# Performance work log

Measured on AMD Instinct MI355X. Metric: run time of the kernel, lower is better.

Reference implementation:

```python
import jax, jax.numpy as jnp
import numpy as np

BS, GRID, LSTM_H, CNN_C, PROJ = 256, 49, 512, 2048, 512


def setup_inputs() -> dict:
    key = jax.random.key(0)
    ks = jax.random.split(key, 7)
    s = lambda fan_in: 1.0 / np.sqrt(fan_in)
    return {
        "lstm_hidden": jax.random.normal(ks[0], (BS, LSTM_H), jnp.float32),
        "cnn_feat": jax.random.normal(ks[1], (BS, GRID, CNN_C), jnp.float32),
        "W_lstm": jax.random.normal(ks[2], (PROJ, LSTM_H), jnp.float32) * s(LSTM_H),
        "b_lstm": jax.random.normal(ks[3], (PROJ,), jnp.float32) * s(LSTM_H),
        "W_cnn": jax.random.normal(ks[4], (PROJ, CNN_C), jnp.float32) * s(CNN_C),
        "b_cnn": jax.random.normal(ks[5], (PROJ,), jnp.float32) * s(CNN_C),
        "w_attn": jax.random.normal(ks[6], (1, PROJ), jnp.float32) * s(PROJ),
    }


def reference(lstm_hidden, cnn_feat, W_lstm, b_lstm, W_cnn, b_cnn, w_attn):
    # H computed once (original loop recomputes it per grid, identically)
    H = lstm_hidden @ W_lstm.T + b_lstm                       # (bs, P)
    V = jnp.einsum("bgc,pc->bgp", cnn_feat, W_cnn) + b_cnn    # (bs, G, P)
    z = jnp.tanh(H[:, None, :] + V) @ w_attn[0]               # (bs, G)
    bs, G = z.shape
    # Faithful to torch: cat over grids along dim 0 -> (G*bs,), then view(bs, G)
    z_scrambled = jnp.swapaxes(z, 0, 1).reshape(bs, G)
    return jax.nn.softmax(z_scrambled, axis=1)
```

## Files before the change

### kernel.cpp

```cpp
#include <hip/hip_runtime.h>
#include <math.h>

#define BSZ    256
#define GRID_N 49
#define LSTMH  512
#define CNN_C  2048
#define PROJ   512
#define KAUG   2560
#define M_TOT  12544
#define MT     64
#define NT     256
#define BK     64
#define KTILES (KAUG / BK)
#define NBLK   ((M_TOT / MT) * (PROJ / NT))

typedef short bf16x8 __attribute__((ext_vector_type(8)));
typedef float f32x4  __attribute__((ext_vector_type(4)));

static __device__ __forceinline__ unsigned short bf16_rne(float f) {
    unsigned int u = __float_as_uint(f);
    u = u + 0x7FFFu + ((u >> 16) & 1u);
    return (unsigned short)(u >> 16);
}
static __device__ __forceinline__ uint4 pack8f(const float* f) {
    uint4 o;
    o.x = (unsigned int)bf16_rne(f[0]) | ((unsigned int)bf16_rne(f[1]) << 16);
    o.y = (unsigned int)bf16_rne(f[2]) | ((unsigned int)bf16_rne(f[3]) << 16);
    o.z = (unsigned int)bf16_rne(f[4]) | ((unsigned int)bf16_rne(f[5]) << 16);
    o.w = (unsigned int)bf16_rne(f[6]) | ((unsigned int)bf16_rne(f[7]) << 16);
    return o;
}
static __device__ __forceinline__ float tanh_fast(float x) {
    float e = __expf(2.f * x);
    return 1.f - 2.f / (e + 1.f);
}
static __device__ __forceinline__ void glds16(const void* g, void* l) {
    __builtin_amdgcn_global_load_lds(
        (const __attribute__((address_space(1))) unsigned int*)g,
        (__attribute__((address_space(3))) unsigned int*)l, 16, 0, 0);
}

__global__ __launch_bounds__(256) void prep_w(const float* __restrict__ Wc,
                                              const float* __restrict__ Wl,
                                              unsigned short* __restrict__ wsW) {
    int c  = blockIdx.x * 256 + threadIdx.x;
    int p  = c / 320;
    int kc = (c % 320) * 8;
    const float* src = (kc < CNN_C) ? (Wc + (size_t)p * CNN_C + kc)
                                    : (Wl + (size_t)p * LSTMH + (kc - CNN_C));
    float f[8];
    *(float4*)&f[0] = ((const float4*)src)[0];
    *(float4*)&f[4] = ((const float4*)src)[1];
    *(uint4*)(wsW + (size_t)p * KAUG + kc) = pack8f(f);
}

template <bool WS>
__global__ __launch_bounds__(256, 2) void gemm_k(
    const float* __restrict__ lstm, const float* __restrict__ cnn,
    const float* __restrict__ Wc,   const float* __restrict__ Wl,
    const float* __restrict__ bl,   const float* __restrict__ bc,
    const float* __restrict__ wat,  const unsigned short* __restrict__ wsW,
    float* __restrict__ out)
{
    __shared__ unsigned short Ash[MT][BK];
    __shared__ unsigned short Bsh[NT][BK];
    __shared__ float zp[4][MT];

    const int t   = threadIdx.x;
    const int w   = t >> 6;
    const int l   = t & 63;
    const int q   = l >> 4;
    const int r16 = l & 15;

    const int m0 = (int)(blockIdx.x >> 1) * MT;
    const int n0 = (int)(blockIdx.x & 1) * NT;

    const int ra  = t >> 2;
    const int ca0 = t & 3;
    const int sa  = ra & 7;
    const int grow = m0 + ra;
    const int ab   = grow / 49;
    const int ag   = grow - ab * 49;
    const float* cnnb  = cnn + ((size_t)ab * GRID_N + ag) * CNN_C;
    const float* lstmb = lstm + (size_t)ab * LSTMH;

    f32x4 acc[4][4];
    #pragma unroll
    for (int mt = 0; mt < 4; ++mt)
        #pragma unroll
        for (int nt = 0; nt < 4; ++nt)
            acc[mt][nt] = (f32x4){0.f, 0.f, 0.f, 0.f};

    float4 fa0, fa1, fa2, fa3;

    auto a_load = [&](int k0) {
        const float* s = (k0 < CNN_C) ? (cnnb + k0) : (lstmb + (k0 - CNN_C));
        const float4* p0 = (const float4*)(s + ca0 * 8);
        const float4* p1 = (const float4*)(s + (ca0 + 4) * 8);
        fa0 = p0[0]; fa1 = p0[1];
        fa2 = p1[0]; fa3 = p1[1];
    };
    auto a_write = [&]() {
        float f[8];
        *(float4*)&f[0] = fa0; *(float4*)&f[4] = fa1;
        *(uint4*)&Ash[ra][(ca0 ^ sa) * 8] = pack8f(f);
        *(float4*)&f[0] = fa2; *(float4*)&f[4] = fa3;
        *(uint4*)&Ash[ra][((ca0 + 4) ^ sa) * 8] = pack8f(f);
    };
    auto b_stage = [&](int k0) {
        if constexpr (WS) {
            const int rsub = l >> 3;
            const int cg   = (l & 7) ^ rsub;
            #pragma unroll
            for (int j = 0; j < 8; ++j) {
                const int rowb = w * 64 + j * 8;
                const unsigned short* g =
                    wsW + (size_t)(n0 + rowb + rsub) * KAUG + k0 + cg * 8;
                glds16(g, &Bsh[rowb][0]);
            }
        } else {
            const float* s = (k0 < CNN_C) ? (Wc + (size_t)(n0 + t) * CNN_C + k0)
                                          : (Wl + (size_t)(n0 + t) * LSTMH + (k0 - CNN_C));
            const int sw = t & 7;
            #pragma unroll
            for (int c = 0; c < 8; ++c) {
                float f[8];
                *(float4*)&f[0] = ((const float4*)(s + c * 8))[0];
                *(float4*)&f[4] = ((const float4*)(s + c * 8))[1];
                *(uint4*)&Bsh[t][(c ^ sw) * 8] = pack8f(f);
            }
        }
    };

    a_load(0);
    a_write();
    b_stage(0);

    for (int kt = 0; kt < KTILES; ++kt) {
        __syncthreads();
        const bool more = (kt + 1 < KTILES);
        if (more) a_load((kt + 1) * BK);
        #pragma unroll
        for (int ks = 0; ks < 2; ++ks) {
            const int cp = ((ks * 4 + q) ^ (r16 & 7)) * 8;
            bf16x8 af[4], bfr[4];
            #pragma unroll
            for (int mt = 0; mt < 4; ++mt)
                af[mt] = *(const bf16x8*)&Ash[mt * 16 + r16][cp];
            #pragma unroll
            for (int nt = 0; nt < 4; ++nt)
                bfr[nt] = *(const bf16x8*)&Bsh[w * 64 + nt * 16 + r16][cp];
            #pragma unroll
            for (int mt = 0; mt < 4; ++mt)
                #pragma unroll
                for (int nt = 0; nt < 4; ++nt)
                    acc[mt][nt] = __builtin_amdgcn_mfma_f32_16x16x32_bf16(
                        af[mt], bfr[nt], acc[mt][nt], 0, 0, 0);
        }
        __syncthreads();
        if (more) { a_write(); b_stage((kt + 1) * BK); }
    }

    float part[4][4];
    #pragma unroll
    for (int mt = 0; mt < 4; ++mt)
        #pragma unroll
        for (int rr = 0; rr < 4; ++rr) part[mt][rr] = 0.f;
    #pragma unroll
    for (int nt = 0; nt < 4; ++nt) {
        const int p = n0 + w * 64 + nt * 16 + r16;
        const float bb = bl[p] + bc[p];
        const float wa = wat[p];
        #pragma unroll
        for (int mt = 0; mt < 4; ++mt)
            #pragma unroll
            for (int rr = 0; rr < 4; ++rr)
                part[mt][rr] += tanh_fast(acc[mt][nt][rr] + bb) * wa;
    }
    #pragma unroll
    for (int mt = 0; mt < 4; ++mt)
        #pragma unroll
        for (int rr = 0; rr < 4; ++rr) {
            float v = part[mt][rr];
            v += __shfl_xor(v, 1);
            v += __shfl_xor(v, 2);
            v += __shfl_xor(v, 4);
            v += __shfl_xor(v, 8);
            if (r16 == 0) zp[w][mt * 16 + q * 4 + rr] = v;
        }
    __syncthreads();
    if (t < MT) {
        const float v = zp[0][t] + zp[1][t] + zp[2][t] + zp[3][t];
        const int row = m0 + t;
        const int b2  = row / 49;
        const int g2  = row - b2 * 49;
        atomicAdd(&out[g2 * BSZ + b2], v);
    }
}

__global__ __launch_bounds__(64) void softmax_rows(float* __restrict__ out)
{
    const int i = blockIdx.x;
    const int j = threadIdx.x;
    float x = (j < GRID_N) ? out[i * GRID_N + j] : -1e30f;
    float m = x;
    #pragma unroll
    for (int off = 32; off > 0; off >>= 1) m = fmaxf(m, __shfl_xor(m, off));
    float e = (j < GRID_N) ? __expf(x - m) : 0.f;
    float s = e;
    #pragma unroll
    for (int off = 32; off > 0; off >>= 1) s += __shfl_xor(s, off);
    if (j < GRID_N) out[i * GRID_N + j] = e / s;
}

extern "C" void kernel_launch(void* const* d_in, const int* in_sizes, int n_in,
                              void* d_out, int out_size, void* d_ws, size_t ws_size,
                              hipStream_t stream)
{
    const float* lstm = (const float*)d_in[0];
    const float* cnn  = (const float*)d_in[1];
    const float* Wl   = (const float*)d_in[2];
    const float* bl   = (const float*)d_in[3];
    const float* Wc   = (const float*)d_in[4];
    const float* bc   = (const float*)d_in[5];
    const float* wat  = (const float*)d_in[6];
    float* out = (float*)d_out;

    hipMemsetAsync(out, 0, (size_t)out_size * sizeof(float), stream);

    const size_t wneed = (size_t)PROJ * KAUG * sizeof(unsigned short);
    if (ws_size >= wneed) {
        unsigned short* wsW = (unsigned short*)d_ws;
        prep_w<<<dim3(640), dim3(256), 0, stream>>>(Wc, Wl, wsW);
        gemm_k<true><<<dim3(NBLK), dim3(256), 0, stream>>>(lstm, cnn, Wc, Wl, bl, bc, wat, wsW, out);
    } else {
        gemm_k<false><<<dim3(NBLK), dim3(256), 0, stream>>>(lstm, cnn, Wc, Wl, bl, bc, wat, nullptr, out);
    }
    softmax_rows<<<dim3(BSZ), dim3(64), 0, stream>>>(out);
}
```

Before: 231.7 us.

## Halve N tile, load B fragments directly to registers, double-buffer A in LDS

The N tile drops from 256 to 128, so four blocks share each M tile and each wave owns 32 columns. B is no longer staged through LDS via global_load_lds. Each lane loads its bf16 weight fragments straight from global memory into a two-stage register buffer. A is double-buffered in LDS with a ping-pong loop unrolled by two, which drops one barrier per k-tile. Occupancy is raised to 3 blocks per SM, at the cost of reading the converted activations (A) twice as often and doing uncoalesced per-lane B loads.

```diff
diff --git a/kernel.cpp b/kernel.cpp
--- a/kernel.cpp
+++ b/kernel.cpp
@@ -9,7 +9,7 @@
 #define KAUG   2560
 #define M_TOT  12544
 #define MT     64
-#define NT     256
+#define NT     128
 #define BK     64
 #define KTILES (KAUG / BK)
 #define NBLK   ((M_TOT / MT) * (PROJ / NT))
@@ -33,11 +33,6 @@
 static __device__ __forceinline__ float tanh_fast(float x) {
     float e = __expf(2.f * x);
     return 1.f - 2.f / (e + 1.f);
-}
-static __device__ __forceinline__ void glds16(const void* g, void* l) {
-    __builtin_amdgcn_global_load_lds(
-        (const __attribute__((address_space(1))) unsigned int*)g,
-        (__attribute__((address_space(3))) unsigned int*)l, 16, 0, 0);
 }
 
 __global__ __launch_bounds__(256) void prep_w(const float* __restrict__ Wc,
@@ -55,15 +50,14 @@
 }
 
 template <bool WS>
-__global__ __launch_bounds__(256, 2) void gemm_k(
+__global__ __launch_bounds__(256, 3) void gemm_k(
     const float* __restrict__ lstm, const float* __restrict__ cnn,
     const float* __restrict__ Wc,   const float* __restrict__ Wl,
     const float* __restrict__ bl,   const float* __restrict__ bc,
     const float* __restrict__ wat,  const unsigned short* __restrict__ wsW,
     float* __restrict__ out)
 {
-    __shared__ unsigned short Ash[MT][BK];
-    __shared__ unsigned short Bsh[NT][BK];
+    __shared__ unsigned short Ash[2][MT][BK];
     __shared__ float zp[4][MT];
 
     const int t   = threadIdx.x;
@@ -72,93 +66,100 @@
     const int q   = l >> 4;
     const int r16 = l & 15;
 
-    const int m0 = (int)(blockIdx.x >> 1) * MT;
-    const int n0 = (int)(blockIdx.x & 1) * NT;
-
-    const int ra  = t >> 2;
-    const int ca0 = t & 3;
-    const int sa  = ra & 7;
+    const int m0 = (int)(blockIdx.x >> 2) * MT;
+    const int n0 = (int)(blockIdx.x & 3) * NT;
+
+    const int ra = t >> 2;
+    const int ca = t & 3;
+    const int sw = ra & 7;
     const int grow = m0 + ra;
     const int ab   = grow / 49;
     const int ag   = grow - ab * 49;
     const float* cnnb  = cnn + ((size_t)ab * GRID_N + ag) * CNN_C;
     const float* lstmb = lstm + (size_t)ab * LSTMH;
 
-    f32x4 acc[4][4];
+    const int bn = n0 + w * 32 + r16;
+    const int bk = q * 8;
+
+    f32x4 acc[4][2];
     #pragma unroll
     for (int mt = 0; mt < 4; ++mt)
         #pragma unroll
-        for (int nt = 0; nt < 4; ++nt)
+        for (int nt = 0; nt < 2; ++nt)
             acc[mt][nt] = (f32x4){0.f, 0.f, 0.f, 0.f};
 
-    float4 fa0, fa1, fa2, fa3;
+    float4 fa[4];
+    bf16x8 Breg[2][2][2];
 
     auto a_load = [&](int k0) {
         const float* s = (k0 < CNN_C) ? (cnnb + k0) : (lstmb + (k0 - CNN_C));
-        const float4* p0 = (const float4*)(s + ca0 * 8);
-        const float4* p1 = (const float4*)(s + (ca0 + 4) * 8);
-        fa0 = p0[0]; fa1 = p0[1];
-        fa2 = p1[0]; fa3 = p1[1];
-    };
-    auto a_write = [&]() {
-        float f[8];
-        *(float4*)&f[0] = fa0; *(float4*)&f[4] = fa1;
-        *(uint4*)&Ash[ra][(ca0 ^ sa) * 8] = pack8f(f);
-        *(float4*)&f[0] = fa2; *(float4*)&f[4] = fa3;
-        *(uint4*)&Ash[ra][((ca0 + 4) ^ sa) * 8] = pack8f(f);
-    };
-    auto b_stage = [&](int k0) {
-        if constexpr (WS) {
-            const int rsub = l >> 3;
-            const int cg   = (l & 7) ^ rsub;
-            #pragma unroll
-            for (int j = 0; j < 8; ++j) {
-                const int rowb = w * 64 + j * 8;
-                const unsigned short* g =
-                    wsW + (size_t)(n0 + rowb + rsub) * KAUG + k0 + cg * 8;
-                glds16(g, &Bsh[rowb][0]);
+        const float4* p = (const float4*)(s + ca * 16);
+        fa[0] = p[0]; fa[1] = p[1]; fa[2] = p[2]; fa[3] = p[3];
+    };
+    auto a_write = [&](int buf) {
+        float f[16];
+        *(float4*)&f[0]  = fa[0]; *(float4*)&f[4]  = fa[1];
+        *(float4*)&f[8]  = fa[2]; *(float4*)&f[12] = fa[3];
+        *(uint4*)&Ash[buf][ra][((2 * ca) ^ sw) * 8]     = pack8f(&f[0]);
+        *(uint4*)&Ash[buf][ra][((2 * ca + 1) ^ sw) * 8] = pack8f(&f[8]);
+    };
+    auto b_load = [&](int k0, int pp) {
+        #pragma unroll
+        for (int nt = 0; nt < 2; ++nt)
+            #pragma unroll
+            for (int ks = 0; ks < 2; ++ks) {
+                if constexpr (WS) {
+                    Breg[pp][nt][ks] = *(const bf16x8*)(
+                        wsW + (size_t)(bn + nt * 16) * KAUG + k0 + ks * 32 + bk);
+                } else {
+                    const int kk = k0 + ks * 32 + bk;
+                    const int n  = bn + nt * 16;
+                    const float* s = (kk < CNN_C) ? (Wc + (size_t)n * CNN_C + kk)
+                                                  : (Wl + (size_t)n * LSTMH + (kk - CNN_C));
+                    float f[8];
+                    *(float4*)&f[0] = ((const float4*)s)[0];
+                    *(float4*)&f[4] = ((const float4*)s)[1];
+                    uint4 u = pack8f(f);
+                    Breg[pp][nt][ks] = *(bf16x8*)&u;
+                }
             }
-        } else {
-            const float* s = (k0 < CNN_C) ? (Wc + (size_t)(n0 + t) * CNN_C + k0)
-                                          : (Wl + (size_t)(n0 + t) * LSTMH + (k0 - CNN_C));
-            const int sw = t & 7;
-            #pragma unroll
-            for (int c = 0; c < 8; ++c) {
-                float f[8];
-                *(float4*)&f[0] = ((const float4*)(s + c * 8))[0];
-                *(float4*)&f[4] = ((const float4*)(s + c * 8))[1];
-                *(uint4*)&Bsh[t][(c ^ sw) * 8] = pack8f(f);
-            }
-        }
-    };
-
-    a_load(0);
-    a_write();
-    b_stage(0);
-
-    for (int kt = 0; kt < KTILES; ++kt) {
-        __syncthreads();
-        const bool more = (kt + 1 < KTILES);
-        if (more) a_load((kt + 1) * BK);
+    };
+    auto compute = [&](int buf, int pp) {
         #pragma unroll
         for (int ks = 0; ks < 2; ++ks) {
             const int cp = ((ks * 4 + q) ^ (r16 & 7)) * 8;
-            bf16x8 af[4], bfr[4];
+            bf16x8 af[4];
             #pragma unroll
             for (int mt = 0; mt < 4; ++mt)
-                af[mt] = *(const bf16x8*)&Ash[mt * 16 + r16][cp];
-            #pragma unroll
-            for (int nt = 0; nt < 4; ++nt)
-                bfr[nt] = *(const bf16x8*)&Bsh[w * 64 + nt * 16 + r16][cp];
+                af[mt] = *(const bf16x8*)&Ash[buf][mt * 16 + r16][cp];
             #pragma unroll
             for (int mt = 0; mt < 4; ++mt)
                 #pragma unroll
-                for (int nt = 0; nt < 4; ++nt)
+                for (int nt = 0; nt < 2; ++nt)
                     acc[mt][nt] = __builtin_amdgcn_mfma_f32_16x16x32_bf16(
-                        af[mt], bfr[nt], acc[mt][nt], 0, 0, 0);
+                        af[mt], Breg[pp][nt][ks], acc[mt][nt], 0, 0, 0);
         }
+    };
+
+    a_load(0);
+    b_load(0, 0);
+    a_write(0);
+    __syncthreads();
+
+    for (int kt = 0; kt < KTILES; kt += 2) {
+        a_load((kt + 1) * BK);
+        b_load((kt + 1) * BK, 1);
+        compute(0, 0);
+        a_write(1);
         __syncthreads();
-        if (more) { a_write(); b_stage((kt + 1) * BK); }
+        const bool more = (kt + 2 < KTILES);
+        if (more) {
+            a_load((kt + 2) * BK);
+            b_load((kt + 2) * BK, 0);
+        }
+        compute(1, 1);
+        if (more) a_write(0);
+        __syncthreads();
     }
 
     float part[4][4];
@@ -167,8 +168,8 @@
         #pragma unroll
         for (int rr = 0; rr < 4; ++rr) part[mt][rr] = 0.f;
     #pragma unroll
-    for (int nt = 0; nt < 4; ++nt) {
-        const int p = n0 + w * 64 + nt * 16 + r16;
+    for (int nt = 0; nt < 2; ++nt) {
+        const int p = n0 + w * 32 + nt * 16 + r16;
         const float bb = bl[p] + bc[p];
         const float wa = wat[p];
         #pragma unroll
```

Result: slower. 283.2 us (+22.3%).

## Double the K tile and register-prefetch B instead of direct-to-LDS loads

Applied to the files above, without the earlier changes.

Raises the K tile from 64 to 128, halving the number of k-iterations and barriers per tile. The weight tile is now prefetched into registers alongside A, overlapping with the MFMA work and written to LDS afterwards, replacing the global_load_lds path. It uses a 16-way XOR swizzle and reuses the A buffer for the reduction scratch. The cost is much higher register pressure (24 extra uint4/float4 per thread), which may reduce occupancy below the 2-block launch bound or cause spills, and doubled LDS use.

```diff
diff --git a/kernel.cpp b/kernel.cpp
--- a/kernel.cpp
+++ b/kernel.cpp
@@ -10,7 +10,7 @@
 #define M_TOT  12544
 #define MT     64
 #define NT     256
-#define BK     64
+#define BK     128
 #define KTILES (KAUG / BK)
 #define NBLK   ((M_TOT / MT) * (PROJ / NT))
 
@@ -33,11 +33,6 @@
 static __device__ __forceinline__ float tanh_fast(float x) {
     float e = __expf(2.f * x);
     return 1.f - 2.f / (e + 1.f);
-}
-static __device__ __forceinline__ void glds16(const void* g, void* l) {
-    __builtin_amdgcn_global_load_lds(
-        (const __attribute__((address_space(1))) unsigned int*)g,
-        (__attribute__((address_space(3))) unsigned int*)l, 16, 0, 0);
 }
 
 __global__ __launch_bounds__(256) void prep_w(const float* __restrict__ Wc,
@@ -64,7 +59,6 @@
 {
     __shared__ unsigned short Ash[MT][BK];
     __shared__ unsigned short Bsh[NT][BK];
-    __shared__ float zp[4][MT];
 
     const int t   = threadIdx.x;
     const int w   = t >> 6;
@@ -76,14 +70,16 @@
     const int n0 = (int)(blockIdx.x & 1) * NT;
 
     const int ra  = t >> 2;
-    const int ca0 = t & 3;
-    const int sa  = ra & 7;
+    const int seg = t & 3;
+    const int swa = ra & 15;
     const int grow = m0 + ra;
     const int ab   = grow / 49;
     const int ag   = grow - ab * 49;
     const float* cnnb  = cnn + ((size_t)ab * GRID_N + ag) * CNN_C;
     const float* lstmb = lstm + (size_t)ab * LSTMH;
 
+    const int swb = t & 15;
+
     f32x4 acc[4][4];
     #pragma unroll
     for (int mt = 0; mt < 4; ++mt)
@@ -91,74 +87,78 @@
         for (int nt = 0; nt < 4; ++nt)
             acc[mt][nt] = (f32x4){0.f, 0.f, 0.f, 0.f};
 
-    float4 fa0, fa1, fa2, fa3;
+    float4 fa[8];
+    uint4  fb[16];
 
     auto a_load = [&](int k0) {
-        const float* s = (k0 < CNN_C) ? (cnnb + k0) : (lstmb + (k0 - CNN_C));
-        const float4* p0 = (const float4*)(s + ca0 * 8);
-        const float4* p1 = (const float4*)(s + (ca0 + 4) * 8);
-        fa0 = p0[0]; fa1 = p0[1];
-        fa2 = p1[0]; fa3 = p1[1];
+        const float* s = ((k0 < CNN_C) ? (cnnb + k0) : (lstmb + (k0 - CNN_C))) + seg * 32;
+        #pragma unroll
+        for (int i = 0; i < 8; ++i) fa[i] = ((const float4*)s)[i];
     };
     auto a_write = [&]() {
-        float f[8];
-        *(float4*)&f[0] = fa0; *(float4*)&f[4] = fa1;
-        *(uint4*)&Ash[ra][(ca0 ^ sa) * 8] = pack8f(f);
-        *(float4*)&f[0] = fa2; *(float4*)&f[4] = fa3;
-        *(uint4*)&Ash[ra][((ca0 + 4) ^ sa) * 8] = pack8f(f);
-    };
-    auto b_stage = [&](int k0) {
+        #pragma unroll
+        for (int j = 0; j < 4; ++j) {
+            float f[8];
+            *(float4*)&f[0] = fa[2 * j];
+            *(float4*)&f[4] = fa[2 * j + 1];
+            const int c = seg * 4 + j;
+            *(uint4*)&Ash[ra][(c ^ swa) * 8] = pack8f(f);
+        }
+    };
+    auto b_load = [&](int k0) {
         if constexpr (WS) {
-            const int rsub = l >> 3;
-            const int cg   = (l & 7) ^ rsub;
-            #pragma unroll
-            for (int j = 0; j < 8; ++j) {
-                const int rowb = w * 64 + j * 8;
-                const unsigned short* g =
-                    wsW + (size_t)(n0 + rowb + rsub) * KAUG + k0 + cg * 8;
-                glds16(g, &Bsh[rowb][0]);
-            }
+            const unsigned short* s = wsW + (size_t)(n0 + t) * KAUG + k0;
+            #pragma unroll
+            for (int c = 0; c < 16; ++c) fb[c] = ((const uint4*)s)[c];
         } else {
             const float* s = (k0 < CNN_C) ? (Wc + (size_t)(n0 + t) * CNN_C + k0)
                                           : (Wl + (size_t)(n0 + t) * LSTMH + (k0 - CNN_C));
-            const int sw = t & 7;
-            #pragma unroll
-            for (int c = 0; c < 8; ++c) {
+            #pragma unroll
+            for (int c = 0; c < 16; ++c) {
                 float f[8];
                 *(float4*)&f[0] = ((const float4*)(s + c * 8))[0];
                 *(float4*)&f[4] = ((const float4*)(s + c * 8))[1];
-                *(uint4*)&Bsh[t][(c ^ sw) * 8] = pack8f(f);
+                fb[c] = pack8f(f);
             }
         }
     };
+    auto b_write = [&]() {
+        #pragma unroll
+        for (int c = 0; c < 16; ++c)
+            *(uint4*)&Bsh[t][(c ^ swb) * 8] = fb[c];
+    };
 
     a_load(0);
+    b_load(0);
     a_write();
-    b_stage(0);
+    b_write();
+    __syncthreads();
 
     for (int kt = 0; kt < KTILES; ++kt) {
-        __syncthreads();
         const bool more = (kt + 1 < KTILES);
-        if (more) a_load((kt + 1) * BK);
-        #pragma unroll
-        for (int ks = 0; ks < 2; ++ks) {
-            const int cp = ((ks * 4 + q) ^ (r16 & 7)) * 8;
-            bf16x8 af[4], bfr[4];
+        if (more) {
+            a_load((kt + 1) * BK);
+            b_load((kt + 1) * BK);
+        }
+        #pragma unroll
+        for (int ks = 0; ks < 4; ++ks) {
+            bf16x8 af[4], bf[4];
             #pragma unroll
             for (int mt = 0; mt < 4; ++mt)
-                af[mt] = *(const bf16x8*)&Ash[mt * 16 + r16][cp];
+                af[mt] = *(const bf16x8*)&Ash[mt * 16 + r16][((ks * 4 + q) ^ r16) * 8];
             #pragma unroll
             for (int nt = 0; nt < 4; ++nt)
-                bfr[nt] = *(const bf16x8*)&Bsh[w * 64 + nt * 16 + r16][cp];
+                bf[nt] = *(const bf16x8*)&Bsh[w * 64 + nt * 16 + r16][((ks * 4 + q) ^ r16) * 8];
             #pragma unroll
             for (int mt = 0; mt < 4; ++mt)
                 #pragma unroll
                 for (int nt = 0; nt < 4; ++nt)
                     acc[mt][nt] = __builtin_amdgcn_mfma_f32_16x16x32_bf16(
-                        af[mt], bfr[nt], acc[mt][nt], 0, 0, 0);
+                        af[mt], bf[nt], acc[mt][nt], 0, 0, 0);
         }
         __syncthreads();
-        if (more) { a_write(); b_stage((kt + 1) * BK); }
+        if (more) { a_write(); b_write(); }
+        __syncthreads();
     }
 
     float part[4][4];
@@ -177,6 +177,7 @@
             for (int rr = 0; rr < 4; ++rr)
                 part[mt][rr] += tanh_fast(acc[mt][nt][rr] + bb) * wa;
     }
+    float (*zp)[MT] = (float (*)[MT])(&Ash[0][0]);
     #pragma unroll
     for (int mt = 0; mt < 4; ++mt)
         #pragma unroll
```

Result: slower. 438.8 us (+89.4%).

## Halve GEMM M-tile, raise occupancy, fuse zeroing and last-block softmax

Applied to the files above, without the earlier changes.

Shrinks the GEMM row tile from 64 to 32 and raises the launch bound from 2 to 4 blocks per CU. This doubles the block count and improves latency hiding while A fp32 loads are converted to bf16. Output zeroing moves into the weight-prep kernel, replacing the separate memset. The softmax is folded into the GEMM through a global atomic completion counter, so the last finishing block normalizes all rows. The trade-offs are more B-tile traffic per output row, an extra barrier per K iteration, and a serial softmax tail in one block.

```diff
diff --git a/kernel.cpp b/kernel.cpp
--- a/kernel.cpp
+++ b/kernel.cpp
@@ -8,11 +8,12 @@
 #define PROJ   512
 #define KAUG   2560
 #define M_TOT  12544
-#define MT     64
+#define MT     32
 #define NT     256
 #define BK     64
 #define KTILES (KAUG / BK)
 #define NBLK   ((M_TOT / MT) * (PROJ / NT))
+#define WOFF   ((size_t)PROJ * KAUG)
 
 typedef short bf16x8 __attribute__((ext_vector_type(8)));
 typedef float f32x4  __attribute__((ext_vector_type(4)));
@@ -42,10 +43,13 @@
 
 __global__ __launch_bounds__(256) void prep_w(const float* __restrict__ Wc,
                                               const float* __restrict__ Wl,
-                                              unsigned short* __restrict__ wsW) {
-    int c  = blockIdx.x * 256 + threadIdx.x;
-    int p  = c / 320;
-    int kc = (c % 320) * 8;
+                                              unsigned short* __restrict__ wsW,
+                                              float* __restrict__ out) {
+    const int gid = blockIdx.x * 256 + threadIdx.x;
+    if (gid < M_TOT) out[gid] = 0.f;
+    if (gid == 0) *(unsigned int*)(wsW + WOFF) = 0u;
+    const int p  = gid / 320;
+    const int kc = (gid % 320) * 8;
     const float* src = (kc < CNN_C) ? (Wc + (size_t)p * CNN_C + kc)
                                     : (Wl + (size_t)p * LSTMH + (kc - CNN_C));
     float f[8];
@@ -55,16 +59,16 @@
 }
 
 template <bool WS>
-__global__ __launch_bounds__(256, 2) void gemm_k(
+__global__ __launch_bounds__(256, 4) void gemm_k(
     const float* __restrict__ lstm, const float* __restrict__ cnn,
     const float* __restrict__ Wc,   const float* __restrict__ Wl,
     const float* __restrict__ bl,   const float* __restrict__ bc,
-    const float* __restrict__ wat,  const unsigned short* __restrict__ wsW,
+    const float* __restrict__ wat,  unsigned short* __restrict__ wsW,
     float* __restrict__ out)
 {
     __shared__ unsigned short Ash[MT][BK];
     __shared__ unsigned short Bsh[NT][BK];
-    __shared__ float zp[4][MT];
+    __shared__ unsigned int fin_old;
 
     const int t   = threadIdx.x;
     const int w   = t >> 6;
@@ -75,37 +79,33 @@
     const int m0 = (int)(blockIdx.x >> 1) * MT;
     const int n0 = (int)(blockIdx.x & 1) * NT;
 
-    const int ra  = t >> 2;
-    const int ca0 = t & 3;
-    const int sa  = ra & 7;
+    const int ra  = t >> 3;
+    const int seg = t & 7;
+    const int swa = ra & 7;
     const int grow = m0 + ra;
     const int ab   = grow / 49;
     const int ag   = grow - ab * 49;
     const float* cnnb  = cnn + ((size_t)ab * GRID_N + ag) * CNN_C;
     const float* lstmb = lstm + (size_t)ab * LSTMH;
 
-    f32x4 acc[4][4];
-    #pragma unroll
-    for (int mt = 0; mt < 4; ++mt)
+    f32x4 acc[2][4];
+    #pragma unroll
+    for (int mt = 0; mt < 2; ++mt)
         #pragma unroll
         for (int nt = 0; nt < 4; ++nt)
             acc[mt][nt] = (f32x4){0.f, 0.f, 0.f, 0.f};
 
-    float4 fa0, fa1, fa2, fa3;
+    float4 fa0, fa1;
 
     auto a_load = [&](int k0) {
-        const float* s = (k0 < CNN_C) ? (cnnb + k0) : (lstmb + (k0 - CNN_C));
-        const float4* p0 = (const float4*)(s + ca0 * 8);
-        const float4* p1 = (const float4*)(s + (ca0 + 4) * 8);
-        fa0 = p0[0]; fa1 = p0[1];
-        fa2 = p1[0]; fa3 = p1[1];
+        const float* s = ((k0 < CNN_C) ? (cnnb + k0) : (lstmb + (k0 - CNN_C))) + seg * 8;
+        fa0 = ((const float4*)s)[0];
+        fa1 = ((const float4*)s)[1];
     };
     auto a_write = [&]() {
         float f[8];
         *(float4*)&f[0] = fa0; *(float4*)&f[4] = fa1;
-        *(uint4*)&Ash[ra][(ca0 ^ sa) * 8] = pack8f(f);
-        *(float4*)&f[0] = fa2; *(float4*)&f[4] = fa3;
-        *(uint4*)&Ash[ra][((ca0 + 4) ^ sa) * 8] = pack8f(f);
+        *(uint4*)&Ash[ra][(seg ^ swa) * 8] = pack8f(f);
     };
     auto b_stage = [&](int k0) {
         if constexpr (WS) {
@@ -135,23 +135,23 @@
     a_load(0);
     a_write();
     b_stage(0);
+    __syncthreads();
 
     for (int kt = 0; kt < KTILES; ++kt) {
-        __syncthreads();
         const bool more = (kt + 1 < KTILES);
         if (more) a_load((kt + 1) * BK);
         #pragma unroll
         for (int ks = 0; ks < 2; ++ks) {
             const int cp = ((ks * 4 + q) ^ (r16 & 7)) * 8;
-            bf16x8 af[4], bfr[4];
-            #pragma unroll
-            for (int mt = 0; mt < 4; ++mt)
+            bf16x8 af[2], bfr[4];
+            #pragma unroll
+            for (int mt = 0; mt < 2; ++mt)
                 af[mt] = *(const bf16x8*)&Ash[mt * 16 + r16][cp];
             #pragma unroll
             for (int nt = 0; nt < 4; ++nt)
                 bfr[nt] = *(const bf16x8*)&Bsh[w * 64 + nt * 16 + r16][cp];
             #pragma unroll
-            for (int mt = 0; mt < 4; ++mt)
+            for (int mt = 0; mt < 2; ++mt)
                 #pragma unroll
                 for (int nt = 0; nt < 4; ++nt)
                     acc[mt][nt] = __builtin_amdgcn_mfma_f32_16x16x32_bf16(
@@ -159,11 +159,12 @@
         }
         __syncthreads();
         if (more) { a_write(); b_stage((kt + 1) * BK); }
-    }
-
-    float part[4][4];
-    #pragma unroll
-    for (int mt = 0; mt < 4; ++mt)
+        __syncthreads();
+    }
+
+    float part[2][4];
+    #pragma unroll
+    for (int mt = 0; mt < 2; ++mt)
         #pragma unroll
         for (int rr = 0; rr < 4; ++rr) part[mt][rr] = 0.f;
     #pragma unroll
@@ -172,13 +173,14 @@
         const float bb = bl[p] + bc[p];
         const float wa = wat[p];
         #pragma unroll
-        for (int mt = 0; mt < 4; ++mt)
+        for (int mt = 0; mt < 2; ++mt)
             #pragma unroll
             for (int rr = 0; rr < 4; ++rr)
                 part[mt][rr] += tanh_fast(acc[mt][nt][rr] + bb) * wa;
     }
-    #pragma unroll
-    for (int mt = 0; mt < 4; ++mt)
+    float (*zp)[MT] = (float (*)[MT])(&Ash[0][0]);
+    #pragma unroll
+    for (int mt = 0; mt < 2; ++mt)
         #pragma unroll
         for (int rr = 0; rr < 4; ++rr) {
             float v = part[mt][rr];
@@ -196,10 +198,43 @@
         const int g2  = row - b2 * 49;
         atomicAdd(&out[g2 * BSZ + b2], v);
     }
-}
-
-__global__ __launch_bounds__(64) void softmax_rows(float* __restrict__ out)
-{
+
+    if constexpr (WS) {
+        __threadfence();
+        __syncthreads();
+        unsigned int* cnt = (unsigned int*)(wsW + WOFF);
+        if (t == 0) fin_old = atomicAdd(cnt, 1u);
+        __syncthreads();
+        if (fin_old == NBLK - 1u) {
+            __threadfence();
+            const size_t base = (size_t)t * GRID_N;
+            float mx = -1e30f;
+            for (int j = 0; j < GRID_N; ++j) {
+                float x = __hip_atomic_load(&out[base + j], __ATOMIC_RELAXED,
+                                            __HIP_MEMORY_SCOPE_AGENT);
+                mx = fmaxf(mx, x);
+            }
+            float s = 0.f;
+            for (int j = 0; j < GRID_N; ++j) {
+                float x = __hip_atomic_load(&out[base + j], __ATOMIC_RELAXED,
+                                            __HIP_MEMORY_SCOPE_AGENT);
+                s += __expf(x - mx);
+            }
+            const float inv = 1.f / s;
+            for (int j = 0; j < GRID_N; ++j) {
+                float x = __hip_atomic_load(&out[base + j], __ATOMIC_RELAXED,
+                                            __HIP_MEMORY_SCOPE_AGENT);
+                out[base + j] = __expf(x - mx) * inv;
+            }
+        }
+    }
+}
+
+__global__ __launch_bounds__(256) void zero_out(float* __restrict__ out) {
+    const int gid = blockIdx.x * 256 + threadIdx.x;
+    if (gid < M_TOT) out[gid] = 0.f;
+}
+__global__ __launch_bounds__(64) void softmax_rows(float* __restrict__ out) {
     const int i = blockIdx.x;
     const int j = threadIdx.x;
     float x = (j < GRID_N) ? out[i * GRID_N + j] : -1e30f;
@@ -226,15 +261,16 @@
     const float* wat  = (const float*)d_in[6];
     float* out = (float*)d_out;
 
-    hipMemsetAsync(out, 0, (size_t)out_size * sizeof(float), stream);
-
-    const size_t wneed = (size_t)PROJ * KAUG * sizeof(unsigned short);
+    const size_t wneed = WOFF * sizeof(unsigned short) + sizeof(unsigned int);
     if (ws_size >= wneed) {
         unsigned short* wsW = (unsigned short*)d_ws;
-        prep_w<<<dim3(640), dim3(256), 0, stream>>>(Wc, Wl, wsW);
-        gemm_k<true><<<dim3(NBLK), dim3(256), 0, stream>>>(lstm, cnn, Wc, Wl, bl, bc, wat, wsW, out);
+        prep_w<<<dim3(640), dim3(256), 0, stream>>>(Wc, Wl, wsW, out);
+        gemm_k<true><<<dim3(NBLK), dim3(256), 0, stream>>>(
+            lstm, cnn, Wc, Wl, bl, bc, wat, wsW, out);
     } else {
-        gemm_k<false><<<dim3(NBLK), dim3(256), 0, stream>>>(lstm, cnn, Wc, Wl, bl, bc, wat, nullptr, out);
-    }
-    softmax_rows<<<dim3(BSZ), dim3(64), 0, stream>>>(out);
-}
+        zero_out<<<dim3(49), dim3(256), 0, stream>>>(out);
+        gemm_k<false><<<dim3(NBLK), dim3(256), 0, stream>>>(
+            lstm, cnn, Wc, Wl, bl, bc, wat, nullptr, out);
+        softmax_rows<<<dim3(BSZ), dim3(64), 0, stream>>>(out);
+    }
+}
```

New measurement: 304.8 us. 1.32x slower.
